# Kernel tuning notes

Measured on AMD Instinct MI355X. Metric: run time of the kernel, lower is better.

The kernel has to match this reference:

```python
import jax, jax.numpy as jnp
import numpy as np

N, E = 100000, 1600000
DN, DE, H = 128, 48, 256
IN = DN + DE  # concat(node_feats, edge_mean_feats) -> 176


def setup_inputs() -> dict:
    key = jax.random.key(0)
    ks = jax.random.split(key, 10)
    return {
        "feature_nodes": jax.random.normal(ks[0], (N, DN), jnp.float32),
        "feature_edges": jax.random.normal(ks[1], (E, DE), jnp.float32),
        "src": jax.random.randint(ks[2], (E,), 0, N, jnp.int32),
        "dst": jax.random.randint(ks[3], (E,), 0, N, jnp.int32),
        "W_self1": jax.random.normal(ks[4], (IN, H), jnp.float32) / np.sqrt(IN).astype(np.float32),
        "W_neigh1": jax.random.normal(ks[5], (IN, H), jnp.float32) / np.sqrt(IN).astype(np.float32),
        "b1": jnp.zeros((H,), jnp.float32),
        "W_self2": jax.random.normal(ks[6], (H, H), jnp.float32) / np.sqrt(H).astype(np.float32),
        "W_neigh2": jax.random.normal(ks[7], (H, H), jnp.float32) / np.sqrt(H).astype(np.float32),
        "b2": jnp.zeros((H,), jnp.float32),
    }


def _seg_mean(vals, idx, n):
    # mean-reduce edge/message values onto destination nodes; zero-degree -> 0
    s = jax.ops.segment_sum(vals, idx, num_segments=n)
    cnt = jax.ops.segment_sum(jnp.ones((vals.shape[0],), vals.dtype), idx, num_segments=n)
    return s / jnp.maximum(cnt, 1.0)[:, None]


def _sage_conv(x, src, dst, W_self, W_neigh, b):
    # DGL SAGEConv 'mean': fc_self(x) + fc_neigh(mean of src-neighbor feats)
    n = x.shape[0]
    h_neigh = _seg_mean(x[src], dst, n)  # gather -> scatter-mean
    return x @ W_self + h_neigh @ W_neigh + b


def reference(feature_nodes, feature_edges, src, dst,
              W_self1, W_neigh1, b1, W_self2, W_neigh2, b2):
    n = feature_nodes.shape[0]
    # g.update_all(copy_e('e','m_e'), mean('m_e','h_e')): mean of incoming edge feats
    h_e = _seg_mean(feature_edges, dst, n)  # [N, DE]
    h = jnp.concatenate([feature_nodes, h_e], axis=1)  # [N, DN+DE]
    h = jax.nn.relu(_sage_conv(h, src, dst, W_self1, W_neigh1, b1))
    h = _sage_conv(h, src, dst, W_self2, W_neigh2, b2)
    return h
```

## Files before the change

kernel.cpp:

```cpp
#include <hip/hip_runtime.h>

#define N_NODES 100000
#define N_EDGES 1600000
#define DN 128
#define DE 48
#define HDIM 256
#define IN1 176
#define K1 352
#define K2 512
#define NPAD 100096
#define NB 391

typedef __bf16 bf16;
typedef __bf16 bf16x2 __attribute__((ext_vector_type(2)));
typedef __bf16 bf16x8 __attribute__((ext_vector_type(8)));
typedef float  f32x4  __attribute__((ext_vector_type(4)));

#define O_DEG  0UL
#define O_ROW  400384UL
#define O_CUR  800768UL
#define O_PRE  1201152UL
#define O_PART 1601536UL
#define O_CSR  1603584UL
#define O_H1   14403584UL
#define O_H2   84871168UL
#define O_W1   187369472UL
#define O_W2   187549696UL

__device__ __forceinline__ float bf_lo(unsigned u) { return __uint_as_float(u << 16); }
__device__ __forceinline__ float bf_hi(unsigned u) { return __uint_as_float(u & 0xffff0000u); }
__device__ __forceinline__ unsigned bf_pk(float a, float b) {
    union { bf16x2 v; unsigned u; } t;
    t.v.x = (bf16)a; t.v.y = (bf16)b;
    return t.u;
}

__global__ void k_prep_weights(const float* __restrict__ Ws1, const float* __restrict__ Wn1,
                               const float* __restrict__ Ws2, const float* __restrict__ Wn2,
                               bf16* __restrict__ Wt1, bf16* __restrict__ Wt2) {
    int tid = blockIdx.x * 256 + threadIdx.x;
    if (tid < HDIM * K1) {
        int n = tid / K1, k = tid - n * K1;
        float v = (k < IN1) ? Ws1[k * HDIM + n] : Wn1[(k - IN1) * HDIM + n];
        Wt1[n * K1 + k] = (bf16)v;
    } else {
        int t2 = tid - HDIM * K1;
        int n = t2 / K2, k = t2 - n * K2;
        float v = (k < HDIM) ? Ws2[k * HDIM + n] : Wn2[(k - HDIM) * HDIM + n];
        Wt2[n * K2 + k] = (bf16)v;
    }
}

__global__ void k_count(const int* __restrict__ dst, int* __restrict__ deg) {
    int e = blockIdx.x * 256 + threadIdx.x;
    if (e < N_EDGES) atomicAdd(&deg[dst[e]], 1);
}

template <int NT>
__device__ __forceinline__ int block_scan_inc(int v, int* lds) {
    int tid = threadIdx.x;
    lds[tid] = v;
#pragma unroll
    for (int off = 1; off < NT; off <<= 1) {
        __syncthreads();
        int t = (tid >= off) ? lds[tid - off] : 0;
        __syncthreads();
        lds[tid] += t;
    }
    return lds[tid];
}

__global__ void k_scanA(const int* __restrict__ deg, int* __restrict__ presum,
                        int* __restrict__ part) {
    __shared__ int lds[256];
    int idx = blockIdx.x * 256 + threadIdx.x;
    int v = (idx < N_NODES) ? deg[idx] : 0;
    int inc = block_scan_inc<256>(v, lds);
    presum[idx] = inc - v;
    if (threadIdx.x == 255) part[blockIdx.x] = inc;
}

__global__ void k_scanB(int* __restrict__ part) {
    __shared__ int lds[512];
    int t = threadIdx.x;
    int v = (t < NB) ? part[t] : 0;
    int inc = block_scan_inc<512>(v, lds);
    if (t < NB) part[t] = inc - v;
}

__global__ void k_scanC(const int* __restrict__ presum, const int* __restrict__ part,
                        int* __restrict__ rowptr, int* __restrict__ cursor) {
    int idx = blockIdx.x * 256 + threadIdx.x;
    int v = presum[idx] + part[blockIdx.x];
    if (idx < N_NODES) { rowptr[idx] = v; cursor[idx] = v; }
}

__global__ void k_fill(const int* __restrict__ src, const int* __restrict__ dst,
                       int* __restrict__ cursor, int2* __restrict__ csr) {
    int e = blockIdx.x * 256 + threadIdx.x;
    int p = atomicAdd(&cursor[dst[e]], 1);
    csr[p] = make_int2(src[e], e);
}


__global__ void k_agg_edges(const float* __restrict__ fn, const float* __restrict__ fe,
                            const int* __restrict__ rowptr, const int* __restrict__ deg,
                            const int2* __restrict__ csr, bf16* __restrict__ h1) {
    int node = blockIdx.x * 4 + (threadIdx.x >> 6);
    int lane = threadIdx.x & 63;
    bf16* row = h1 + (size_t)node * K1;
    float2 f = *(const float2*)(fn + (size_t)node * DN + lane * 2);
    *(unsigned*)&row[lane * 2] = bf_pk(f.x, f.y);
    int base = rowptr[node], d = deg[node];
    int slot = lane / 12;
    int sub  = lane - slot * 12;
    bool act = lane < 48;
    f32x4 s = {0.f, 0.f, 0.f, 0.f};
    for (int c = 0; c < d; c += 64) {
        int nn = min(d - c, 64);
        int myE = (lane < nn) ? csr[base + c + lane].y : 0;
        for (int i = 0; i < nn; i += 16) {
            f32x4 v[4];
#pragma unroll
            for (int g = 0; g < 4; ++g) {
                int ei = i + g * 4 + slot;
                int e = __shfl(myE, ei);
                v[g] = (f32x4){0.f, 0.f, 0.f, 0.f};
                if (act && ei < nn)
                    v[g] = *(const f32x4*)(fe + (size_t)e * DE + sub * 4);
            }
            s += (v[0] + v[1]) + (v[2] + v[3]);
        }
    }
#pragma unroll
    for (int k = 0; k < 4; ++k) {
        float t = s[k];
        t += __shfl(s[k], lane + 12);
        t += __shfl(s[k], lane + 24);
        t += __shfl(s[k], lane + 36);
        s[k] = t;
    }
    if (lane < 12) {
        float r = 1.0f / (float)max(d, 1);
        uint2 o;
        o.x = bf_pk(s[0] * r, s[1] * r);
        o.y = bf_pk(s[2] * r, s[3] * r);
        *((uint2*)(row + DN) + lane) = o;
    }
}

__global__ void k_agg1(const int* __restrict__ rowptr, const int* __restrict__ deg,
                       const int2* __restrict__ csr, bf16* __restrict__ h1) {
    int node = blockIdx.x * 4 + (threadIdx.x >> 6);
    int lane = threadIdx.x & 63;
    int base = rowptr[node], d = deg[node];
    int slot = (lane < 22) ? 0 : ((lane < 44) ? 1 : 2);
    int sub  = lane - slot * 22;
    bool act = lane < 44;
    float s0 = 0.f, s1 = 0.f, s2 = 0.f, s3 = 0.f, s4 = 0.f, s5 = 0.f, s6 = 0.f, s7 = 0.f;
    for (int c = 0; c < d; c += 64) {
        int nn = min(d - c, 64);
        int mySv = (lane < nn) ? csr[base + c + lane].x : 0;
        for (int i = 0; i < nn; i += 16) {
            uint4 q[8];
#pragma unroll
            for (int g = 0; g < 8; ++g) {
                int ei = i + g * 2 + slot;
                int sv = __shfl(mySv, ei);
                q[g] = make_uint4(0u, 0u, 0u, 0u);
                if (act && ei < nn)
                    q[g] = *((const uint4*)(h1 + (size_t)sv * K1) + sub);
            }
#pragma unroll
            for (int g = 0; g < 8; ++g) {
                s0 += bf_lo(q[g].x); s1 += bf_hi(q[g].x);
                s2 += bf_lo(q[g].y); s3 += bf_hi(q[g].y);
                s4 += bf_lo(q[g].z); s5 += bf_hi(q[g].z);
                s6 += bf_lo(q[g].w); s7 += bf_hi(q[g].w);
            }
        }
    }
    s0 += __shfl(s0, lane + 22); s1 += __shfl(s1, lane + 22);
    s2 += __shfl(s2, lane + 22); s3 += __shfl(s3, lane + 22);
    s4 += __shfl(s4, lane + 22); s5 += __shfl(s5, lane + 22);
    s6 += __shfl(s6, lane + 22); s7 += __shfl(s7, lane + 22);
    if (lane < 22) {
        float r = 1.0f / (float)max(d, 1);
        uint4 o;
        o.x = bf_pk(s0 * r, s1 * r);
        o.y = bf_pk(s2 * r, s3 * r);
        o.z = bf_pk(s4 * r, s5 * r);
        o.w = bf_pk(s6 * r, s7 * r);
        *((uint4*)(h1 + (size_t)node * K1 + IN1) + lane) = o;
    }
}

__global__ void k_agg2(const int* __restrict__ rowptr, const int* __restrict__ deg,
                       const int2* __restrict__ csr, bf16* __restrict__ h2) {
    int node = blockIdx.x * 4 + (threadIdx.x >> 6);
    int lane = threadIdx.x & 63;
    int base = rowptr[node], d = deg[node];
    int half = lane >> 5, sub = lane & 31;
    float s0 = 0.f, s1 = 0.f, s2 = 0.f, s3 = 0.f, s4 = 0.f, s5 = 0.f, s6 = 0.f, s7 = 0.f;
    for (int c = 0; c < d; c += 64) {
        int nn = min(d - c, 64);
        int mySv = (lane < nn) ? csr[base + c + lane].x : 0;
        for (int i = 0; i < nn; i += 16) {
            uint4 q[8];
#pragma unroll
            for (int g = 0; g < 8; ++g) {
                int ei = i + g * 2 + half;
                int sv = __shfl(mySv, ei);
                q[g] = make_uint4(0u, 0u, 0u, 0u);
                if (ei < nn)
                    q[g] = *((const uint4*)(h2 + (size_t)sv * K2) + sub);
            }
#pragma unroll
            for (int g = 0; g < 8; ++g) {
                s0 += bf_lo(q[g].x); s1 += bf_hi(q[g].x);
                s2 += bf_lo(q[g].y); s3 += bf_hi(q[g].y);
                s4 += bf_lo(q[g].z); s5 += bf_hi(q[g].z);
                s6 += bf_lo(q[g].w); s7 += bf_hi(q[g].w);
            }
        }
    }
    s0 += __shfl(s0, lane ^ 32); s1 += __shfl(s1, lane ^ 32);
    s2 += __shfl(s2, lane ^ 32); s3 += __shfl(s3, lane ^ 32);
    s4 += __shfl(s4, lane ^ 32); s5 += __shfl(s5, lane ^ 32);
    s6 += __shfl(s6, lane ^ 32); s7 += __shfl(s7, lane ^ 32);
    if (half == 0) {
        float r = 1.0f / (float)max(d, 1);
        uint4 o;
        o.x = bf_pk(s0 * r, s1 * r);
        o.y = bf_pk(s2 * r, s3 * r);
        o.z = bf_pk(s4 * r, s5 * r);
        o.w = bf_pk(s6 * r, s7 * r);
        *((uint4*)(h2 + (size_t)node * K2 + HDIM) + sub) = o;
    }
}

template <bool RELU, typename OT>
__global__ __launch_bounds__(256) void k_gemm(const bf16* __restrict__ A,
                                              const bf16* __restrict__ Wt,
                                              const float* __restrict__ bias,
                                              OT* __restrict__ out,
                                              int Ktiles, int ostride) {
    __shared__ __align__(16) bf16 lA[128 * 40];
    __shared__ __align__(16) bf16 lB[128 * 40];

    const int tid = threadIdx.x;
    const int rowBase = blockIdx.x * 128;
    const int colBase = blockIdx.y * 128;
    const int l = tid & 63, w = tid >> 6;
    const int wr = (w >> 1) * 64, wc = (w & 1) * 64;
    const int lm = l & 15, lq = l >> 4;
    const int K = Ktiles * 32;

    const int srow = tid >> 1;
    const int sko  = (tid & 1) * 16;

    const bf16* pA = A  + (size_t)(rowBase + srow) * K + sko;
    const bf16* pB = Wt + (size_t)(colBase + srow) * K + sko;

    f32x4 acc[4][4] = {};

    uint4 a0 = *(const uint4*)(pA), a1 = *(const uint4*)(pA + 8);
    uint4 b0 = *(const uint4*)(pB), b1 = *(const uint4*)(pB + 8);

    for (int kt = 0; kt < Ktiles; ++kt) {
        __syncthreads();
        *(uint4*)&lA[srow * 40 + sko]     = a0;
        *(uint4*)&lA[srow * 40 + sko + 8] = a1;
        *(uint4*)&lB[srow * 40 + sko]     = b0;
        *(uint4*)&lB[srow * 40 + sko + 8] = b1;
        __syncthreads();

        if (kt + 1 < Ktiles) {
            pA += 32; pB += 32;
            a0 = *(const uint4*)(pA); a1 = *(const uint4*)(pA + 8);
            b0 = *(const uint4*)(pB); b1 = *(const uint4*)(pB + 8);
        }

        bf16x8 af[4], bfr[4];
#pragma unroll
        for (int mi = 0; mi < 4; ++mi)
            af[mi] = *(const bf16x8*)&lA[(wr + mi * 16 + lm) * 40 + lq * 8];
#pragma unroll
        for (int ni = 0; ni < 4; ++ni)
            bfr[ni] = *(const bf16x8*)&lB[(wc + ni * 16 + lm) * 40 + lq * 8];
#pragma unroll
        for (int mi = 0; mi < 4; ++mi)
#pragma unroll
            for (int ni = 0; ni < 4; ++ni)
                acc[mi][ni] = __builtin_amdgcn_mfma_f32_16x16x32_bf16(
                    af[mi], bfr[ni], acc[mi][ni], 0, 0, 0);
    }

#pragma unroll
    for (int ni = 0; ni < 4; ++ni) {
        const int gcol = colBase + wc + ni * 16 + lm;
        const float bv = bias[gcol];
#pragma unroll
        for (int mi = 0; mi < 4; ++mi) {
#pragma unroll
            for (int r = 0; r < 4; ++r) {
                const int grow = rowBase + wr + mi * 16 + lq * 4 + r;
                if (grow < N_NODES) {
                    float v = acc[mi][ni][r] + bv;
                    if (RELU) v = fmaxf(v, 0.0f);
                    out[(size_t)grow * ostride + gcol] = (OT)v;
                }
            }
        }
    }
}

extern "C" void kernel_launch(void* const* d_in, const int* in_sizes, int n_in,
                              void* d_out, int out_size, void* d_ws, size_t ws_size,
                              hipStream_t stream) {
    const float* fn  = (const float*)d_in[0];
    const float* fe  = (const float*)d_in[1];
    const int*   src = (const int*)d_in[2];
    const int*   dst = (const int*)d_in[3];
    const float* Ws1 = (const float*)d_in[4];
    const float* Wn1 = (const float*)d_in[5];
    const float* b1  = (const float*)d_in[6];
    const float* Ws2 = (const float*)d_in[7];
    const float* Wn2 = (const float*)d_in[8];
    const float* b2  = (const float*)d_in[9];
    float* out = (float*)d_out;

    char* ws = (char*)d_ws;
    int*  deg    = (int*)(ws + O_DEG);
    int*  rowptr = (int*)(ws + O_ROW);
    int*  cursor = (int*)(ws + O_CUR);
    int*  presum = (int*)(ws + O_PRE);
    int*  part   = (int*)(ws + O_PART);
    int2* csr    = (int2*)(ws + O_CSR);
    bf16* h1  = (bf16*)(ws + O_H1);
    bf16* h2  = (bf16*)(ws + O_H2);
    bf16* Wt1 = (bf16*)(ws + O_W1);
    bf16* Wt2 = (bf16*)(ws + O_W2);

    hipMemsetAsync(deg, 0, (size_t)NPAD * 4, stream);
    hipMemsetAsync((char*)h1 + (size_t)N_NODES * K1 * 2, 0, (size_t)(NPAD - N_NODES) * K1 * 2, stream);
    hipMemsetAsync((char*)h2 + (size_t)N_NODES * K2 * 2, 0, (size_t)(NPAD - N_NODES) * K2 * 2, stream);

    k_prep_weights<<<(HDIM * K1 + HDIM * K2) / 256, 256, 0, stream>>>(Ws1, Wn1, Ws2, Wn2, Wt1, Wt2);

    k_count<<<(N_EDGES + 255) / 256, 256, 0, stream>>>(dst, deg);
    k_scanA<<<NB, 256, 0, stream>>>(deg, presum, part);
    k_scanB<<<1, 512, 0, stream>>>(part);
    k_scanC<<<NB, 256, 0, stream>>>(presum, part, rowptr, cursor);
    k_fill<<<N_EDGES / 256, 256, 0, stream>>>(src, dst, cursor, csr);

    k_agg_edges<<<N_NODES / 4, 256, 0, stream>>>(fn, fe, rowptr, deg, csr, h1);
    k_agg1<<<N_NODES / 4, 256, 0, stream>>>(rowptr, deg, csr, h1);
    k_gemm<true, bf16><<<dim3(NPAD / 128, 2), 256, 0, stream>>>(h1, Wt1, b1, h2, K1 / 32, K2);

    k_agg2<<<N_NODES / 4, 256, 0, stream>>>(rowptr, deg, csr, h2);
    k_gemm<false, float><<<dim3(NPAD / 128, 2), 256, 0, stream>>>(h2, Wt2, b2, out, K2 / 32, HDIM);
}
```

Baseline: 1.032 ms.

## Fuse neighbor aggregation into GEMM via LDS-staged mean features

Replaces the separate aggregation kernels and the GEMMs with one fused kernel per layer. Each block first gathers the neighbor means for its 128 rows into swizzled LDS, then runs MFMA over the self features (read straight from global) and the LDS neighbor tile. The padded layouts (192/256 columns instead of 352/512) drop the concatenated h buffers, cutting global write and read traffic. In exchange, each wave aggregates 32 nodes serially with only 782 blocks, the B operand is loaded from global without LDS reuse, and the gather phase cannot overlap with the MFMA phase, so occupancy and latency hiding may suffer.

```diff
diff --git a/kernel.cpp b/kernel.cpp
--- a/kernel.cpp
+++ b/kernel.cpp
@@ -5,9 +5,7 @@
 #define DN 128
 #define DE 48
 #define HDIM 256
-#define IN1 176
-#define K1 352
-#define K2 512
+#define KX 192
 #define NPAD 100096
 #define NB 391
 
@@ -22,10 +20,10 @@
 #define O_PRE  1201152UL
 #define O_PART 1601536UL
 #define O_CSR  1603584UL
-#define O_H1   14403584UL
-#define O_H2   84871168UL
-#define O_W1   187369472UL
-#define O_W2   187549696UL
+#define O_X    14403584UL
+#define O_H2A  52840448UL
+#define O_W1   104089600UL
+#define O_W2   104286208UL
 
 __device__ __forceinline__ float bf_lo(unsigned u) { return __uint_as_float(u << 16); }
 __device__ __forceinline__ float bf_hi(unsigned u) { return __uint_as_float(u & 0xffff0000u); }
@@ -39,15 +37,17 @@
                                const float* __restrict__ Ws2, const float* __restrict__ Wn2,
                                bf16* __restrict__ Wt1, bf16* __restrict__ Wt2) {
     int tid = blockIdx.x * 256 + threadIdx.x;
-    if (tid < HDIM * K1) {
-        int n = tid / K1, k = tid - n * K1;
-        float v = (k < IN1) ? Ws1[k * HDIM + n] : Wn1[(k - IN1) * HDIM + n];
-        Wt1[n * K1 + k] = (bf16)v;
+    if (tid < HDIM * 384) {
+        int n = tid / 384, k = tid - n * 384;
+        float v = 0.0f;
+        if (k < 176) v = Ws1[k * HDIM + n];
+        else if (k >= 192 && k < 368) v = Wn1[(k - 192) * HDIM + n];
+        Wt1[n * 384 + k] = (bf16)v;
     } else {
-        int t2 = tid - HDIM * K1;
-        int n = t2 / K2, k = t2 - n * K2;
+        int t2 = tid - HDIM * 384;
+        int n = t2 / 512, k = t2 - n * 512;
         float v = (k < HDIM) ? Ws2[k * HDIM + n] : Wn2[(k - HDIM) * HDIM + n];
-        Wt2[n * K2 + k] = (bf16)v;
+        Wt2[n * 512 + k] = (bf16)v;
     }
 }
 
@@ -92,7 +92,7 @@
                         int* __restrict__ rowptr, int* __restrict__ cursor) {
     int idx = blockIdx.x * 256 + threadIdx.x;
     int v = presum[idx] + part[blockIdx.x];
-    if (idx < N_NODES) { rowptr[idx] = v; cursor[idx] = v; }
+    rowptr[idx] = v; cursor[idx] = v;
 }
 
 __global__ void k_fill(const int* __restrict__ src, const int* __restrict__ dst,
@@ -102,13 +102,12 @@
     csr[p] = make_int2(src[e], e);
 }
 
-
 __global__ void k_agg_edges(const float* __restrict__ fn, const float* __restrict__ fe,
                             const int* __restrict__ rowptr, const int* __restrict__ deg,
-                            const int2* __restrict__ csr, bf16* __restrict__ h1) {
+                            const int2* __restrict__ csr, bf16* __restrict__ x) {
     int node = blockIdx.x * 4 + (threadIdx.x >> 6);
     int lane = threadIdx.x & 63;
-    bf16* row = h1 + (size_t)node * K1;
+    bf16* row = x + (size_t)node * KX;
     float2 f = *(const float2*)(fn + (size_t)node * DN + lane * 2);
     *(unsigned*)&row[lane * 2] = bf_pk(f.x, f.y);
     int base = rowptr[node], d = deg[node];
@@ -146,169 +145,119 @@
         o.x = bf_pk(s[0] * r, s[1] * r);
         o.y = bf_pk(s[2] * r, s[3] * r);
         *((uint2*)(row + DN) + lane) = o;
-    }
-}
-
-__global__ void k_agg1(const int* __restrict__ rowptr, const int* __restrict__ deg,
-                       const int2* __restrict__ csr, bf16* __restrict__ h1) {
-    int node = blockIdx.x * 4 + (threadIdx.x >> 6);
-    int lane = threadIdx.x & 63;
-    int base = rowptr[node], d = deg[node];
-    int slot = (lane < 22) ? 0 : ((lane < 44) ? 1 : 2);
-    int sub  = lane - slot * 22;
-    bool act = lane < 44;
-    float s0 = 0.f, s1 = 0.f, s2 = 0.f, s3 = 0.f, s4 = 0.f, s5 = 0.f, s6 = 0.f, s7 = 0.f;
-    for (int c = 0; c < d; c += 64) {
-        int nn = min(d - c, 64);
-        int mySv = (lane < nn) ? csr[base + c + lane].x : 0;
-        for (int i = 0; i < nn; i += 16) {
-            uint4 q[8];
-#pragma unroll
-            for (int g = 0; g < 8; ++g) {
-                int ei = i + g * 2 + slot;
-                int sv = __shfl(mySv, ei);
-                q[g] = make_uint4(0u, 0u, 0u, 0u);
-                if (act && ei < nn)
-                    q[g] = *((const uint4*)(h1 + (size_t)sv * K1) + sub);
+    } else if (lane < 16) {
+        *((uint2*)(row + DN) + lane) = make_uint2(0u, 0u);
+    }
+}
+
+template <int KST, int KS, int LPE, bool RELU, typename OT>
+__global__ __launch_bounds__(256, 2) void k_fused(const bf16* __restrict__ X,
+                                                  const bf16* __restrict__ Wt,
+                                                  const float* __restrict__ bias,
+                                                  const int* __restrict__ rowptr,
+                                                  const int* __restrict__ deg,
+                                                  const int2* __restrict__ csr,
+                                                  OT* __restrict__ out) {
+    constexpr int K = 2 * KST * 32;
+    __shared__ __align__(16) bf16 nb[KST * 128 * 32];
+
+    const int tid = threadIdx.x;
+    const int lane = tid & 63, wq = tid >> 6;
+    const int rowBase = blockIdx.x * 128;
+
+    {
+        int slot, sub; bool act;
+        if (LPE == 32) { slot = lane >> 5; sub = lane & 31; act = true; }
+        else { slot = (lane < LPE) ? 0 : ((lane < 2 * LPE) ? 1 : 2); sub = lane - slot * LPE; act = (slot < 2); }
+        for (int nl = 0; nl < 32; ++nl) {
+            int node = rowBase + wq * 32 + nl;
+            int base = rowptr[node], d = deg[node];
+            float s[8] = {0.f, 0.f, 0.f, 0.f, 0.f, 0.f, 0.f, 0.f};
+            for (int c = 0; c < d; c += 64) {
+                int nn = min(d - c, 64);
+                int mySv = (lane < nn) ? csr[base + c + lane].x : 0;
+                for (int i = 0; i < nn; i += 16) {
+                    uint4 q[8];
+#pragma unroll
+                    for (int g = 0; g < 8; ++g) {
+                        int ei = i + g * 2 + slot;
+                        int sv = __shfl(mySv, ei);
+                        q[g] = make_uint4(0u, 0u, 0u, 0u);
+                        if (act && ei < nn)
+                            q[g] = *((const uint4*)(X + (size_t)sv * KS) + sub);
+                    }
+#pragma unroll
+                    for (int g = 0; g < 8; ++g) {
+                        s[0] += bf_lo(q[g].x); s[1] += bf_hi(q[g].x);
+                        s[2] += bf_lo(q[g].y); s[3] += bf_hi(q[g].y);
+                        s[4] += bf_lo(q[g].z); s[5] += bf_hi(q[g].z);
+                        s[6] += bf_lo(q[g].w); s[7] += bf_hi(q[g].w);
+                    }
+                }
             }
 #pragma unroll
-            for (int g = 0; g < 8; ++g) {
-                s0 += bf_lo(q[g].x); s1 += bf_hi(q[g].x);
-                s2 += bf_lo(q[g].y); s3 += bf_hi(q[g].y);
-                s4 += bf_lo(q[g].z); s5 += bf_hi(q[g].z);
-                s6 += bf_lo(q[g].w); s7 += bf_hi(q[g].w);
+            for (int k = 0; k < 8; ++k) s[k] += __shfl(s[k], lane + LPE);
+            if (lane < LPE) {
+                float r = 1.0f / (float)max(d, 1);
+                uint4 o;
+                o.x = bf_pk(s[0] * r, s[1] * r);
+                o.y = bf_pk(s[2] * r, s[3] * r);
+                o.z = bf_pk(s[4] * r, s[5] * r);
+                o.w = bf_pk(s[6] * r, s[7] * r);
+                int row = wq * 32 + nl;
+                int kc = sub >> 2, lqw = sub & 3;
+                *(uint4*)&nb[kc * 4096 + row * 32 + 8 * (lqw ^ (row & 3))] = o;
             }
         }
     }
-    s0 += __shfl(s0, lane + 22); s1 += __shfl(s1, lane + 22);
-    s2 += __shfl(s2, lane + 22); s3 += __shfl(s3, lane + 22);
-    s4 += __shfl(s4, lane + 22); s5 += __shfl(s5, lane + 22);
-    s6 += __shfl(s6, lane + 22); s7 += __shfl(s7, lane + 22);
-    if (lane < 22) {
-        float r = 1.0f / (float)max(d, 1);
-        uint4 o;
-        o.x = bf_pk(s0 * r, s1 * r);
-        o.y = bf_pk(s2 * r, s3 * r);
-        o.z = bf_pk(s4 * r, s5 * r);
-        o.w = bf_pk(s6 * r, s7 * r);
-        *((uint4*)(h1 + (size_t)node * K1 + IN1) + lane) = o;
-    }
-}
-
-__global__ void k_agg2(const int* __restrict__ rowptr, const int* __restrict__ deg,
-                       const int2* __restrict__ csr, bf16* __restrict__ h2) {
-    int node = blockIdx.x * 4 + (threadIdx.x >> 6);
-    int lane = threadIdx.x & 63;
-    int base = rowptr[node], d = deg[node];
-    int half = lane >> 5, sub = lane & 31;
-    float s0 = 0.f, s1 = 0.f, s2 = 0.f, s3 = 0.f, s4 = 0.f, s5 = 0.f, s6 = 0.f, s7 = 0.f;
-    for (int c = 0; c < d; c += 64) {
-        int nn = min(d - c, 64);
-        int mySv = (lane < nn) ? csr[base + c + lane].x : 0;
-        for (int i = 0; i < nn; i += 16) {
-            uint4 q[8];
-#pragma unroll
-            for (int g = 0; g < 8; ++g) {
-                int ei = i + g * 2 + half;
-                int sv = __shfl(mySv, ei);
-                q[g] = make_uint4(0u, 0u, 0u, 0u);
-                if (ei < nn)
-                    q[g] = *((const uint4*)(h2 + (size_t)sv * K2) + sub);
-            }
-#pragma unroll
-            for (int g = 0; g < 8; ++g) {
-                s0 += bf_lo(q[g].x); s1 += bf_hi(q[g].x);
-                s2 += bf_lo(q[g].y); s3 += bf_hi(q[g].y);
-                s4 += bf_lo(q[g].z); s5 += bf_hi(q[g].z);
-                s6 += bf_lo(q[g].w); s7 += bf_hi(q[g].w);
-            }
-        }
-    }
-    s0 += __shfl(s0, lane ^ 32); s1 += __shfl(s1, lane ^ 32);
-    s2 += __shfl(s2, lane ^ 32); s3 += __shfl(s3, lane ^ 32);
-    s4 += __shfl(s4, lane ^ 32); s5 += __shfl(s5, lane ^ 32);
-    s6 += __shfl(s6, lane ^ 32); s7 += __shfl(s7, lane ^ 32);
-    if (half == 0) {
-        float r = 1.0f / (float)max(d, 1);
-        uint4 o;
-        o.x = bf_pk(s0 * r, s1 * r);
-        o.y = bf_pk(s2 * r, s3 * r);
-        o.z = bf_pk(s4 * r, s5 * r);
-        o.w = bf_pk(s6 * r, s7 * r);
-        *((uint4*)(h2 + (size_t)node * K2 + HDIM) + sub) = o;
-    }
-}
-
-template <bool RELU, typename OT>
-__global__ __launch_bounds__(256) void k_gemm(const bf16* __restrict__ A,
-                                              const bf16* __restrict__ Wt,
-                                              const float* __restrict__ bias,
-                                              OT* __restrict__ out,
-                                              int Ktiles, int ostride) {
-    __shared__ __align__(16) bf16 lA[128 * 40];
-    __shared__ __align__(16) bf16 lB[128 * 40];
-
-    const int tid = threadIdx.x;
-    const int rowBase = blockIdx.x * 128;
-    const int colBase = blockIdx.y * 128;
-    const int l = tid & 63, w = tid >> 6;
-    const int wr = (w >> 1) * 64, wc = (w & 1) * 64;
-    const int lm = l & 15, lq = l >> 4;
-    const int K = Ktiles * 32;
-
-    const int srow = tid >> 1;
-    const int sko  = (tid & 1) * 16;
-
-    const bf16* pA = A  + (size_t)(rowBase + srow) * K + sko;
-    const bf16* pB = Wt + (size_t)(colBase + srow) * K + sko;
-
-    f32x4 acc[4][4] = {};
-
-    uint4 a0 = *(const uint4*)(pA), a1 = *(const uint4*)(pA + 8);
-    uint4 b0 = *(const uint4*)(pB), b1 = *(const uint4*)(pB + 8);
-
-    for (int kt = 0; kt < Ktiles; ++kt) {
-        __syncthreads();
-        *(uint4*)&lA[srow * 40 + sko]     = a0;
-        *(uint4*)&lA[srow * 40 + sko + 8] = a1;
-        *(uint4*)&lB[srow * 40 + sko]     = b0;
-        *(uint4*)&lB[srow * 40 + sko + 8] = b1;
-        __syncthreads();
-
-        if (kt + 1 < Ktiles) {
-            pA += 32; pB += 32;
-            a0 = *(const uint4*)(pA); a1 = *(const uint4*)(pA + 8);
-            b0 = *(const uint4*)(pB); b1 = *(const uint4*)(pB + 8);
-        }
-
-        bf16x8 af[4], bfr[4];
+    __syncthreads();
+
+    const int wr = (wq & 1) * 64, wc = (wq >> 1) * 128;
+    const int lm = lane & 15, lq = lane >> 4;
+    f32x4 acc[4][8] = {};
+
+    for (int kt = 0; kt < KST; ++kt) {
+        bf16x8 af[4];
 #pragma unroll
         for (int mi = 0; mi < 4; ++mi)
-            af[mi] = *(const bf16x8*)&lA[(wr + mi * 16 + lm) * 40 + lq * 8];
-#pragma unroll
-        for (int ni = 0; ni < 4; ++ni)
-            bfr[ni] = *(const bf16x8*)&lB[(wc + ni * 16 + lm) * 40 + lq * 8];
-#pragma unroll
-        for (int mi = 0; mi < 4; ++mi)
-#pragma unroll
-            for (int ni = 0; ni < 4; ++ni)
-                acc[mi][ni] = __builtin_amdgcn_mfma_f32_16x16x32_bf16(
-                    af[mi], bfr[ni], acc[mi][ni], 0, 0, 0);
-    }
-
-#pragma unroll
-    for (int ni = 0; ni < 4; ++ni) {
-        const int gcol = colBase + wc + ni * 16 + lm;
-        const float bv = bias[gcol];
+            af[mi] = *(const bf16x8*)&X[(size_t)(rowBase + wr + mi * 16 + lm) * KS + kt * 32 + lq * 8];
+#pragma unroll
+        for (int ni = 0; ni < 8; ++ni) {
+            bf16x8 bv = *(const bf16x8*)&Wt[(size_t)(wc + ni * 16 + lm) * K + kt * 32 + lq * 8];
+#pragma unroll
+            for (int mi = 0; mi < 4; ++mi)
+                acc[mi][ni] = __builtin_amdgcn_mfma_f32_16x16x32_bf16(af[mi], bv, acc[mi][ni], 0, 0, 0);
+        }
+    }
+    for (int kt = 0; kt < KST; ++kt) {
+        bf16x8 af[4];
 #pragma unroll
         for (int mi = 0; mi < 4; ++mi) {
-#pragma unroll
-            for (int r = 0; r < 4; ++r) {
-                const int grow = rowBase + wr + mi * 16 + lq * 4 + r;
+            int row = wr + mi * 16 + lm;
+            af[mi] = *(const bf16x8*)&nb[kt * 4096 + row * 32 + 8 * (lq ^ (row & 3))];
+        }
+#pragma unroll
+        for (int ni = 0; ni < 8; ++ni) {
+            bf16x8 bv = *(const bf16x8*)&Wt[(size_t)(wc + ni * 16 + lm) * K + (KST + kt) * 32 + lq * 8];
+#pragma unroll
+            for (int mi = 0; mi < 4; ++mi)
+                acc[mi][ni] = __builtin_amdgcn_mfma_f32_16x16x32_bf16(af[mi], bv, acc[mi][ni], 0, 0, 0);
+        }
+    }
+
+#pragma unroll
+    for (int ni = 0; ni < 8; ++ni) {
+        const int gcol = wc + ni * 16 + lm;
+        const float bvv = bias[gcol];
+#pragma unroll
+        for (int mi = 0; mi < 4; ++mi) {
+#pragma unroll
+            for (int r2 = 0; r2 < 4; ++r2) {
+                const int grow = rowBase + wr + mi * 16 + lq * 4 + r2;
                 if (grow < N_NODES) {
-                    float v = acc[mi][ni][r] + bv;
+                    float v = acc[mi][ni][r2] + bvv;
                     if (RELU) v = fmaxf(v, 0.0f);
-                    out[(size_t)grow * ostride + gcol] = (OT)v;
+                    out[(size_t)grow * HDIM + gcol] = (OT)v;
                 }
             }
         }
@@ -337,16 +286,16 @@
     int*  presum = (int*)(ws + O_PRE);
     int*  part   = (int*)(ws + O_PART);
     int2* csr    = (int2*)(ws + O_CSR);
-    bf16* h1  = (bf16*)(ws + O_H1);
-    bf16* h2  = (bf16*)(ws + O_H2);
+    bf16* x   = (bf16*)(ws + O_X);
+    bf16* h2a = (bf16*)(ws + O_H2A);
     bf16* Wt1 = (bf16*)(ws + O_W1);
     bf16* Wt2 = (bf16*)(ws + O_W2);
 
     hipMemsetAsync(deg, 0, (size_t)NPAD * 4, stream);
-    hipMemsetAsync((char*)h1 + (size_t)N_NODES * K1 * 2, 0, (size_t)(NPAD - N_NODES) * K1 * 2, stream);
-    hipMemsetAsync((char*)h2 + (size_t)N_NODES * K2 * 2, 0, (size_t)(NPAD - N_NODES) * K2 * 2, stream);
-
-    k_prep_weights<<<(HDIM * K1 + HDIM * K2) / 256, 256, 0, stream>>>(Ws1, Wn1, Ws2, Wn2, Wt1, Wt2);
+    hipMemsetAsync((char*)x   + (size_t)N_NODES * KX * 2,   0, (size_t)(NPAD - N_NODES) * KX * 2, stream);
+    hipMemsetAsync((char*)h2a + (size_t)N_NODES * HDIM * 2, 0, (size_t)(NPAD - N_NODES) * HDIM * 2, stream);
+
+    k_prep_weights<<<(HDIM * 384 + HDIM * 512) / 256, 256, 0, stream>>>(Ws1, Wn1, Ws2, Wn2, Wt1, Wt2);
 
     k_count<<<(N_EDGES + 255) / 256, 256, 0, stream>>>(dst, deg);
     k_scanA<<<NB, 256, 0, stream>>>(deg, presum, part);
@@ -354,10 +303,9 @@
     k_scanC<<<NB, 256, 0, stream>>>(presum, part, rowptr, cursor);
     k_fill<<<N_EDGES / 256, 256, 0, stream>>>(src, dst, cursor, csr);
 
-    k_agg_edges<<<N_NODES / 4, 256, 0, stream>>>(fn, fe, rowptr, deg, csr, h1);
-    k_agg1<<<N_NODES / 4, 256, 0, stream>>>(rowptr, deg, csr, h1);
-    k_gemm<true, bf16><<<dim3(NPAD / 128, 2), 256, 0, stream>>>(h1, Wt1, b1, h2, K1 / 32, K2);
-
-    k_agg2<<<N_NODES / 4, 256, 0, stream>>>(rowptr, deg, csr, h2);
-    k_gemm<false, float><<<dim3(NPAD / 128, 2), 256, 0, stream>>>(h2, Wt2, b2, out, K2 / 32, HDIM);
-}
+    k_agg_edges<<<N_NODES / 4, 256, 0, stream>>>(fn, fe, rowptr, deg, csr, x);
+
+    k_fused<6, KX, 24, true, bf16><<<NPAD / 128, 256, 0, stream>>>(x, Wt1, b1, rowptr, deg, csr, h2a);
+
+    k_fused<8, HDIM, 32, false, float><<<NPAD / 128, 256, 0, stream>>>(h2a, Wt2, b2, rowptr, deg, csr, out);
+}
```

New measurement: 1.162 ms. +12.6%, slower.
